# Performance work log

Hardware: AMD Instinct MI355X
Metric: run time of the kernel (lower is better)

Reference implementation:

```python
import jax
import jax.numpy as jnp
import numpy as np
from jax import lax

DELTA = float(np.exp(-2.0))  # rule-creation density threshold


def codebook_lamb(x):
    """Online growing RBF prototype codebook (ALMMo-style) for one layer.

    x: [N, M]. Returns lamb: [N] normalized density of each sample at its
    assigned rule. Faithful (corrected) semantics of Layer.__call__:
      - SEN = squared L2 norm per sample (over feature dim)
      - global mean / mean squared norm over the batch
      - sequential per-sample: if max RBF density over existing rules < exp(-2),
        append a new rule (prototype=c=x, SENc=||x||^2, support=1);
        else update rule_star. Note the source's `support[rule_star] = +1`
        assigns 1, so the running mean update degenerates to c[rule_star]=x,
        SENc[rule_star]=||x||^2 -- replicated here.
      - distances use the (never-updated) prototypes; bandwidth stau uses c.
    """
    N, M = x.shape
    SENx = jnp.sum(x * x, axis=-1)                      # [N]
    gmean = jnp.mean(x, axis=0)                         # [M]
    base = jnp.mean(SENx) - jnp.sum(gmean * gmean)      # SENgmean - SEN(gmean)
    R = N                                               # worst case: one rule/sample

    protos0 = jnp.zeros((R, M), x.dtype)
    pn20 = jnp.zeros((R,), x.dtype)                     # ||proto_r||^2 (carried)
    c0 = jnp.zeros((R, M), x.dtype)
    cn20 = jnp.zeros((R,), x.dtype)                     # ||c_r||^2 (carried)
    SENc0 = jnp.zeros((R,), x.dtype)
    count0 = jnp.int32(0)

    ridx = jnp.arange(R)

    def step(carry, inp):
        protos, pn2, c, cn2, SENc, count = carry
        xi, sxi = inp                                   # [M], scalar
        valid = ridx < count
        stau = (base + SENc - cn2) * 0.5                # [R]
        dist = sxi + pn2 - 2.0 * (protos @ xi)          # [R] ||xi - proto_r||^2
        dens = jnp.where(valid, jnp.exp(-dist / stau), -jnp.inf)
        idx = jnp.argmax(dens)
        vmax = dens[idx]
        new = (count == 0) | (vmax < DELTA)
        slot = jnp.where(new, count, idx)
        # both branches set c/SENc at slot to xi/sxi (support resets to 1)
        c = c.at[slot].set(xi)
        cn2 = cn2.at[slot].set(sxi)
        SENc = SENc.at[slot].set(sxi)
        # only a new rule writes a prototype (OOB scatter when count==R is dropped)
        protos = protos.at[count].set(jnp.where(new, xi, protos[count]))
        pn2 = pn2.at[count].set(jnp.where(new, sxi, pn2[count]))
        count = count + new.astype(count.dtype)
        return (protos, pn2, c, cn2, SENc, count), slot

    (protos, pn2, c, cn2, SENc, count), rules = lax.scan(
        step, (protos0, pn20, c0, cn20, SENc0, count0), (x, SENx)
    )

    # final densities of all samples under all (valid) rules: [R, N]
    stau = (base + SENc - cn2) * 0.5                    # [R]
    dist = SENx[None, :] + pn2[:, None] - 2.0 * (protos @ x.T)
    dens = jnp.where((ridx < count)[:, None], jnp.exp(-dist / stau[:, None]), 0.0)
    dens_xn = dens[rules, jnp.arange(N)]                # density at assigned rule
    lamb = dens_xn / jnp.sum(dens, axis=0)              # normalize over rules
    return lamb


def setup_inputs() -> dict:
    key = jax.random.key(0)
    k = jax.random.split(key, 5)
    N, D_IN, D_H, D_OUT = 2048, 2048, 2048, 1024
    s0 = 1.0 / np.sqrt(D_IN)
    s1 = 1.0 / np.sqrt(D_H)
    return {
        "x": jax.random.normal(k[0], (N, D_IN), jnp.float32),
        "W0": jax.random.normal(k[1], (D_H, D_IN), jnp.float32) * s0,
        "b0": jax.random.normal(k[2], (D_H,), jnp.float32) * s0,
        "W1": jax.random.normal(k[3], (D_OUT, D_H), jnp.float32) * s1,
        "b1": jax.random.normal(k[4], (D_OUT,), jnp.float32) * s1,
    }


def reference(x, W0, b0, W1, b1):
    lambs = []
    h = x
    for W, b in ((W0, b0), (W1, b1)):
        lambs.append(codebook_lamb(h))          # per-layer codebook on layer input
        h = jax.nn.sigmoid(h @ W.T + b)         # torch.nn.Linear + sigmoid
    return h, jnp.stack(lambs)                  # ([N, d_out], [n_layers, N])
```

## Files before the change

### kernel.cpp

```cpp
#include <hip/hip_runtime.h>
#include <cstdint>
#include <cstddef>


#define DELTA_F 0.13533528323661270f
#define MBYTE (1u << 20)

typedef __bf16 bf16;
typedef bf16 bf16x8 __attribute__((ext_vector_type(8)));
typedef bf16 bf16x4 __attribute__((ext_vector_type(4)));
typedef float f32x4 __attribute__((ext_vector_type(4)));

typedef __attribute__((address_space(1))) void as1_void;
typedef __attribute__((address_space(3))) void as3_void;

__device__ __forceinline__ void gload16(const bf16* g, bf16* l) {
  __builtin_amdgcn_global_load_lds((as1_void*)g, (as3_void*)l, 16, 0, 0);
}

__device__ __forceinline__ float wave_reduce(float s) {
  for (int o = 32; o > 0; o >>= 1) s += __shfl_down(s, o, 64);
  return s;
}

template <bool SAME>
__device__ void run_decide_lamb(char* smem, int* e, float* Dens, float* S,
                                float* diagD, float* lambOut) {
  char* s_flag = smem;
  short* s_as = (short*)(smem + 2048);
  short* s_list = (short*)(smem + 6144);
  short* s_re = (short*)(smem + 10240);
  int* scan_ = (int*)(smem + 14336);
  float* rbest = (float*)(smem + 16384);
  int* rbj = (int*)(smem + 18432);
  int* sT = (int*)(smem + 24576);
  int* sReN = (int*)(smem + 24580);
  const int tid = threadIdx.x;
  int cntl = 0;
#pragma unroll
  for (int k = 0; k < 4; ++k) {
    const int i = tid * 4 + k;
    const int ei = SAME ? atomicOr(e + i, 0) : e[i];
    s_flag[i] = (ei == 0);
    if (ei == 0) s_as[i] = (short)i;
    cntl += (ei != 0);
  }
  scan_[tid] = cntl;
  if (tid == 0) sReN[0] = 0;
  __syncthreads();
  for (int off = 1; off < 512; off <<= 1) {
    const int v = scan_[tid];
    const int add = (tid >= off) ? scan_[tid - off] : 0;
    __syncthreads();
    scan_[tid] = v + add;
    __syncthreads();
  }
  int pos = scan_[tid] - cntl;
#pragma unroll
  for (int k = 0; k < 4; ++k) {
    const int i = tid * 4 + k;
    if (!s_flag[i]) s_list[pos++] = (short)i;
  }
  if (tid == 511) sT[0] = scan_[511];
  __syncthreads();
  const int T = sT[0];
  if (SAME && T > 0) __threadfence();
  for (int t = 0; t < T; ++t) {
    const int i = s_list[t];
    const float* di = Dens + (size_t)i * 2048;
    float best = -1.0f;
    int bestj = 0x7fffffff;
    for (int j = tid; j < i; j += 512) {
      if (s_flag[j]) {
        const float d = di[j];
        if (d > best || (d == best && j < bestj)) { best = d; bestj = j; }
      }
    }
    rbest[tid] = best; rbj[tid] = bestj;
    __syncthreads();
    if (tid == 0) {
      float b = -1.0f;
      int bj = 0x7fffffff;
      for (int k = 0; k < 512; ++k)
        if (rbest[k] > b || (rbest[k] == b && rbj[k] < bj)) { b = rbest[k]; bj = rbj[k]; }
      if (b < DELTA_F) { s_flag[i] = 1; s_as[i] = (short)i; }
      else { s_as[i] = (short)bj; s_re[sReN[0]++] = (short)i; }
    }
    __syncthreads();
  }
  const int reN = sReN[0];
#pragma unroll
  for (int k = 0; k < 4; ++k) {
    const int n = k * 512 + tid;
    const int aa = s_as[n];
    const float num = (aa == n)
        ? (SAME ? atomicAdd(diagD + n, 0.f) : diagD[n])
        : Dens[(size_t)n * 2048 + aa];
    float denom = SAME ? atomicAdd(S + n, 0.f) : S[n];
    for (int t = 0; t < reN; ++t) denom -= Dens[(size_t)n * 2048 + s_re[t]];
    lambOut[n] = num / denom;
  }
}

template <bool IS_L0>
__global__ __launch_bounds__(512, 2) void gemm_fused(
    const bf16* __restrict__ A, float* __restrict__ Dens,
    bf16* __restrict__ Hb, float* __restrict__ Fo,
    const float* __restrict__ bias, const float* __restrict__ SENin,
    const float* __restrict__ ninv_p, float* __restrict__ S,
    int* __restrict__ e, float* __restrict__ SENhOut,
    float* __restrict__ colsumH, float* __restrict__ diagD,
    int* __restrict__ cnt, int nblocks, float* __restrict__ lambOut,
    int* __restrict__ flagN, const float* __restrict__ SENh_r,
    const float* __restrict__ colsumH_r, int* __restrict__ e0,
    float* __restrict__ S0, float* __restrict__ diag0,
    float* __restrict__ Dens0, float* __restrict__ lamb0) {
  __shared__ __align__(16) char smemA[49152];
  __shared__ __align__(16) char smemB[49152];
  __shared__ __align__(16) char smemC[49152];
  __shared__ int s_last;
  const int tid = threadIdx.x;

  if (!IS_L0 && blockIdx.x == 24) {
    if (blockIdx.y != 0) return;
    float* r1 = (float*)(smemA + 20480);
    float* r2 = (float*)(smemA + 22528);
    float ssen = 0.f, sg2 = 0.f;
    for (int i = tid; i < 2048; i += 512) ssen += SENh_r[i];
    for (int c = tid; c < 2048; c += 512) {
      const float gm = colsumH_r[c] * (1.f / 2048.f);
      sg2 += gm * gm;
    }
    r1[tid] = ssen; r2[tid] = sg2;
    __syncthreads();
    for (int s = 256; s; s >>= 1) {
      if (tid < s) { r1[tid] += r1[tid + s]; r2[tid] += r2[tid + s]; }
      __syncthreads();
    }
    if (tid == 0) {
      const float stau = 0.5f * (r1[0] * (1.f / 2048.f) - r2[0]);
      atomicExch(flagN, __float_as_int(-1.f / stau));
    }
    __syncthreads();
    run_decide_lamb<false>(smemA, e0, Dens0, S0, diag0, lamb0);
    return;
  }

  int bx, by;
  if (IS_L0) {
    const int lid = blockIdx.x + (blockIdx.y << 5);
    by = lid & 7; bx = lid >> 3;
  } else {
    const int lid = blockIdx.x + blockIdx.y * 25;
    const int xcd = lid & 7, j = lid >> 3;
    by = xcd; bx = j - (j > 3 * (xcd + 1));
  }
  const int m0 = by * 256, n0 = bx * 128;

  const int wave = tid >> 6, lane = tid & 63;
  const int quad = lane >> 4, l16 = lane & 15;
  const int wm = wave >> 1, wn = wave & 1;
  const bool isGram = (n0 < 2048);
  const int sr8 = lane >> 3, slot = lane & 7;
  const int gk = (slot ^ sr8) * 8;
  const bf16* aSrc = A + (size_t)(m0 + wave * 32 + sr8) * 2048 + gk;
  const bf16* bSrc = A + (size_t)(n0 + wave * 16 + sr8) * 2048 + gk;
  char* const aDstA = smemA + wave * 4096;
  char* const bDstA = smemA + 32768 + wave * 2048;
  char* const aDstB = smemB + wave * 4096;
  char* const bDstB = smemB + 32768 + wave * 2048;
  char* const aDstC = smemC + wave * 4096;
  char* const bDstC = smemC + 32768 + wave * 2048;
  const int aB = (wm * 64 + l16) * 128;
  const int bB = 32768 + (wn * 64 + l16) * 128;

#define STAGE(aD, bD, k)                                    \
  do {                                                      \
    gload16(aSrc + (k), (bf16*)(aD));                       \
    gload16(aSrc + 8 * 2048 + (k), (bf16*)((aD) + 1024));   \
    gload16(aSrc + 16 * 2048 + (k), (bf16*)((aD) + 2048));  \
    gload16(aSrc + 24 * 2048 + (k), (bf16*)((aD) + 3072));  \
    gload16(bSrc + (k), (bf16*)(bD));                       \
    gload16(bSrc + 8 * 2048 + (k), (bf16*)((bD) + 1024));   \
  } while (0)

#define COMPUTE(sm)                                                          \
  do {                                                                       \
    _Pragma("unroll") for (int ks = 0; ks < 2; ++ks) {                       \
      bf16x8 af[4], bfr[4];                                                  \
      const int sw = ((ks * 4 + quad) ^ (l16 & 7)) * 16;                     \
      _Pragma("unroll") for (int i = 0; i < 4; ++i)                          \
          af[i] = *(const bf16x8*)((sm) + aB + i * 2048 + sw);               \
      _Pragma("unroll") for (int j = 0; j < 4; ++j)                          \
          bfr[j] = *(const bf16x8*)((sm) + bB + j * 2048 + sw);              \
      _Pragma("unroll") for (int i = 0; i < 4; ++i)                          \
          _Pragma("unroll") for (int j = 0; j < 4; ++j) acc[i][j] =          \
              __builtin_amdgcn_mfma_f32_16x16x32_bf16(af[i], bfr[j],         \
                                                      acc[i][j], 0, 0, 0);   \
    }                                                                        \
  } while (0)

#define WBAR(n)                                                  \
  do {                                                           \
    asm volatile("s_waitcnt vmcnt(" #n ")" ::: "memory");        \
    __builtin_amdgcn_sched_barrier(0);                           \
    __builtin_amdgcn_s_barrier();                                \
    __builtin_amdgcn_sched_barrier(0);                           \
  } while (0)

  f32x4 acc[4][4] = {};
  STAGE(aDstA, bDstA, 0);
  STAGE(aDstB, bDstB, 64);
  for (int k0 = 0; k0 < 1920; k0 += 192) {
    WBAR(6); STAGE(aDstC, bDstC, k0 + 128); COMPUTE(smemA);
    WBAR(6); STAGE(aDstA, bDstA, k0 + 192); COMPUTE(smemB);
    WBAR(6); STAGE(aDstB, bDstB, k0 + 256); COMPUTE(smemC);
  }
  WBAR(6); COMPUTE(smemA);
  WBAR(0); COMPUTE(smemB);
#undef STAGE
#undef COMPUTE
#undef WBAR

  float ninv = 0.f;
  if (isGram) {
    if (IS_L0) ninv = ninv_p[0];
    else {
      int fi;
      while ((fi = atomicOr(flagN, 0)) == 0) {}
      ninv = __int_as_float(fi);
    }
  }

  float colp[4] = {0.f, 0.f, 0.f, 0.f};
#pragma unroll
  for (int i = 0; i < 4; ++i) {
    const int rbase = m0 + wm * 64 + i * 16 + quad * 4;
    if (isGram) {
      const f32x4 si4 = *(const f32x4*)(SENin + rbase);
      float rp[4] = {0.f, 0.f, 0.f, 0.f};
      int er = 0;
#pragma unroll
      for (int j = 0; j < 4; ++j) {
        const f32x4 v = acc[i][j];
        const int col = n0 + wn * 64 + j * 16 + l16;
        const float sj = SENin[col];
#pragma unroll
        for (int r = 0; r < 4; ++r) {
          const float dens = __expf((si4[r] + sj - 2.0f * v[r]) * ninv);
          Dens[(size_t)(rbase + r) * 2048 + col] = dens;
          rp[r] += dens;
          if (col < rbase + r && dens >= DELTA_F) er |= (1 << r);
          if (col == rbase + r) atomicExch(diagD + col, dens);
        }
      }
#pragma unroll
      for (int r = 0; r < 4; ++r) {
        float rv = rp[r];
        rv += __shfl_xor(rv, 1, 64); rv += __shfl_xor(rv, 2, 64);
        rv += __shfl_xor(rv, 4, 64); rv += __shfl_xor(rv, 8, 64);
        if (l16 == 0) atomicAdd(S + rbase + r, rv);
      }
      er |= __shfl_xor(er, 1, 64); er |= __shfl_xor(er, 2, 64);
      er |= __shfl_xor(er, 4, 64); er |= __shfl_xor(er, 8, 64);
      if (l16 == 0 && er) {
#pragma unroll
        for (int r = 0; r < 4; ++r)
          if ((er >> r) & 1) atomicOr(e + rbase + r, 1);
      }
    } else {
      float rn[4] = {0.f, 0.f, 0.f, 0.f};
#pragma unroll
      for (int j = 0; j < 4; ++j) {
        const f32x4 v = acc[i][j];
        const int c2 = n0 - 2048 + wn * 64 + j * 16 + l16;
        const float bv = bias[c2];
#pragma unroll
        for (int r = 0; r < 4; ++r) {
          const float hv = 1.0f / (1.0f + __expf(-(v[r] + bv)));
          if (IS_L0) {
            Hb[(size_t)(rbase + r) * 2048 + c2] = (bf16)hv;
            rn[r] += hv * hv;
            colp[j] += hv;
          } else {
            Fo[(size_t)(rbase + r) * 1024 + c2] = hv;
          }
        }
      }
      if (IS_L0) {
#pragma unroll
        for (int r = 0; r < 4; ++r) {
          float rv = rn[r];
          rv += __shfl_xor(rv, 1, 64); rv += __shfl_xor(rv, 2, 64);
          rv += __shfl_xor(rv, 4, 64); rv += __shfl_xor(rv, 8, 64);
          if (l16 == 0) atomicAdd(SENhOut + rbase + r, rv);
        }
      }
    }
  }
  if (IS_L0 && !isGram) {
#pragma unroll
    for (int j = 0; j < 4; ++j) {
      float cv = colp[j];
      cv += __shfl_xor(cv, 16, 64);
      cv += __shfl_xor(cv, 32, 64);
      if (lane < 16) atomicAdd(colsumH + (n0 - 2048 + wn * 64 + j * 16 + lane), cv);
    }
  }

  if (IS_L0) return;

  __syncthreads();
  if (tid == 0) s_last = (atomicAdd(cnt, 1) == nblocks - 1);
  __syncthreads();
  if (!s_last) return;
  run_decide_lamb<true>(smemA, e, Dens, S, diagD, lambOut);
}

__global__ void f2b_all(const float* __restrict__ x, const float* __restrict__ W0,
                        const float* __restrict__ W1, bf16* __restrict__ xb,
                        bf16* __restrict__ wb0, bf16* __restrict__ wb1,
                        float* __restrict__ SENx, float* __restrict__ bins,
                        int* __restrict__ cntF, float* __restrict__ scal) {
  const int b = blockIdx.x, tid = threadIdx.x;
  const int wave = tid >> 6, lane = tid & 63;
  __shared__ float ws[8][4];
  __shared__ float red1[256], red2[256];
  __shared__ int s_last;
  if (b < 256) {
    const int r0 = b * 8;
    f32x4 c0 = {0.f, 0.f, 0.f, 0.f}, c1 = {0.f, 0.f, 0.f, 0.f};
    for (int r = 0; r < 8; ++r) {
      const float* src = x + (size_t)(r0 + r) * 2048;
      bf16* dst = xb + (size_t)(r0 + r) * 2048;
      f32x4 v0 = *(const f32x4*)(src + tid * 4);
      f32x4 v1 = *(const f32x4*)(src + 1024 + tid * 4);
      bf16x4 o0, o1;
      o0.x = (bf16)v0.x; o0.y = (bf16)v0.y; o0.z = (bf16)v0.z; o0.w = (bf16)v0.w;
      o1.x = (bf16)v1.x; o1.y = (bf16)v1.y; o1.z = (bf16)v1.z; o1.w = (bf16)v1.w;
      *(bf16x4*)(dst + tid * 4) = o0;
      *(bf16x4*)(dst + 1024 + tid * 4) = o1;
      c0 += v0; c1 += v1;
      float rn = v0.x * v0.x + v0.y * v0.y + v0.z * v0.z + v0.w * v0.w +
                 v1.x * v1.x + v1.y * v1.y + v1.z * v1.z + v1.w * v1.w;
      rn = wave_reduce(rn);
      if (lane == 0) ws[r][wave] = rn;
    }
    __syncthreads();
    if (tid < 8)
      atomicExch(SENx + r0 + tid, ws[tid][0] + ws[tid][1] + ws[tid][2] + ws[tid][3]);
    float* bin = bins + (size_t)(b & 15) * 2048;
    atomicAdd(bin + tid * 4 + 0, c0.x); atomicAdd(bin + tid * 4 + 1, c0.y);
    atomicAdd(bin + tid * 4 + 2, c0.z); atomicAdd(bin + tid * 4 + 3, c0.w);
    atomicAdd(bin + 1024 + tid * 4 + 0, c1.x); atomicAdd(bin + 1024 + tid * 4 + 1, c1.y);
    atomicAdd(bin + 1024 + tid * 4 + 2, c1.z); atomicAdd(bin + 1024 + tid * 4 + 3, c1.w);
  } else if (b < 512) {
    const size_t base = (size_t)(b - 256) * 16384;
    for (int c = tid * 4; c < 16384; c += 1024) {
      f32x4 v = *(const f32x4*)(W0 + base + c);
      bf16x4 o;
      o.x = (bf16)v.x; o.y = (bf16)v.y; o.z = (bf16)v.z; o.w = (bf16)v.w;
      *(bf16x4*)(wb0 + base + c) = o;
    }
  } else {
    const size_t base = (size_t)(b - 512) * 16384;
    for (int c = tid * 4; c < 16384; c += 1024) {
      f32x4 v = *(const f32x4*)(W1 + base + c);
      bf16x4 o;
      o.x = (bf16)v.x; o.y = (bf16)v.y; o.z = (bf16)v.z; o.w = (bf16)v.w;
      *(bf16x4*)(wb1 + base + c) = o;
    }
  }

  __syncthreads();
  if (tid == 0) s_last = (atomicAdd(cntF, 1) == 639);
  __syncthreads();
  if (!s_last) return;
  float ssen = 0.f;
  for (int i = tid; i < 2048; i += 256) ssen += atomicAdd(SENx + i, 0.f);
  float sg2 = 0.f;
  for (int c = tid; c < 2048; c += 256) {
    float cs = 0.f;
#pragma unroll
    for (int p = 0; p < 16; ++p) cs += atomicAdd(bins + (size_t)p * 2048 + c, 0.f);
    const float gm = cs * (1.f / 2048.f);
    sg2 += gm * gm;
  }
  red1[tid] = ssen; red2[tid] = sg2;
  __syncthreads();
  for (int s = 128; s; s >>= 1) {
    if (tid < s) { red1[tid] += red1[tid + s]; red2[tid] += red2[tid + s]; }
    __syncthreads();
  }
  if (tid == 0) {
    const float stau = 0.5f * (red1[0] * (1.f / 2048.f) - red2[0]);
    scal[0] = stau;
    scal[1] = -1.f / stau;
  }
}

extern "C" void kernel_launch(void* const* d_in, const int* in_sizes, int n_in,
                              void* d_out, int out_size, void* d_ws, size_t ws_size,
                              hipStream_t stream) {
  const float* x = (const float*)d_in[0];
  const float* W0 = (const float*)d_in[1];
  const float* b0 = (const float*)d_in[2];
  const float* W1 = (const float*)d_in[3];
  const float* b1 = (const float*)d_in[4];
  float* out = (float*)d_out;

  char* w = (char*)d_ws;
  bf16* xb = (bf16*)(w);
  bf16* wb0 = (bf16*)(w + 8 * MBYTE);
  bf16* hb = (bf16*)(w + 16 * MBYTE);
  bf16* wb1 = (bf16*)(w + 24 * MBYTE);
  float* Dens0 = (float*)(w + 28 * MBYTE);
  float* Dens1 = (float*)(w);
  float* SENx = (float*)(w + 44 * MBYTE);
  float* scal = SENx + 2048;
  float* zre = scal + 16;
  float* bins = zre;
  float* SENh = bins + 16 * 2048;
  float* colsumH = SENh + 2048;
  float* S0 = colsumH + 2048;
  float* S1 = S0 + 2048;
  float* diagD0 = S1 + 2048;
  float* diagD1 = diagD0 + 2048;
  int* e0 = (int*)(diagD1 + 2048);
  int* e1 = e0 + 2048;
  int* cntF = e1 + 2048;
  int* cnt1 = cntF + 1;
  int* flagN = cnt1 + 1;
  const size_t zwords = 16 * 2048 + 8 * 2048 + 16;

  float* lamb0 = out + (size_t)2048 * 1024;
  float* lamb1 = lamb0 + 2048;

  hipMemsetAsync(zre, 0, zwords * 4, stream);
  f2b_all<<<640, 256, 0, stream>>>(x, W0, W1, xb, wb0, wb1, SENx, bins, cntF, scal);
  gemm_fused<true><<<dim3(32, 8), 512, 0, stream>>>(
      xb, Dens0, hb, nullptr, b0, SENx, scal + 1, S0, e0, SENh, colsumH,
      diagD0, nullptr, 0, nullptr,
      nullptr, nullptr, nullptr, nullptr, nullptr, nullptr, nullptr, nullptr);
  gemm_fused<false><<<dim3(25, 8), 512, 0, stream>>>(
      hb, Dens1, nullptr, out, b1, SENh, nullptr, S1, e1, nullptr, nullptr,
      diagD1, cnt1, 192, lamb1,
      flagN, SENh, colsumH, e0, S0, diagD0, Dens0, lamb0);
}
```

Baseline: 189.9 us.

## Load GEMM B operand directly into registers instead of staging through LDS

The B tile is no longer staged in LDS. Each wave now loads its B fragments straight from global memory into double-buffered registers, one phase ahead, while A keeps its three-stage LDS pipeline and the LDS buffers shrink to 32KB each. The aim is to cut LDS traffic and the LDS read instructions for B, and to lower LDS use. In exchange it adds register pressure, and B is fetched redundantly from global/L2, since each row is loaded by every wave that uses it rather than once per block.

```diff
diff --git a/kernel.cpp b/kernel.cpp
--- a/kernel.cpp
+++ b/kernel.cpp
@@ -115,9 +115,9 @@
     const float* __restrict__ colsumH_r, int* __restrict__ e0,
     float* __restrict__ S0, float* __restrict__ diag0,
     float* __restrict__ Dens0, float* __restrict__ lamb0) {
-  __shared__ __align__(16) char smemA[49152];
-  __shared__ __align__(16) char smemB[49152];
-  __shared__ __align__(16) char smemC[49152];
+  __shared__ __align__(16) char smemA[32768];
+  __shared__ __align__(16) char smemB[32768];
+  __shared__ __align__(16) char smemC[32768];
   __shared__ int s_last;
   const int tid = threadIdx.x;
 
@@ -164,38 +164,52 @@
   const int sr8 = lane >> 3, slot = lane & 7;
   const int gk = (slot ^ sr8) * 8;
   const bf16* aSrc = A + (size_t)(m0 + wave * 32 + sr8) * 2048 + gk;
-  const bf16* bSrc = A + (size_t)(n0 + wave * 16 + sr8) * 2048 + gk;
   char* const aDstA = smemA + wave * 4096;
-  char* const bDstA = smemA + 32768 + wave * 2048;
   char* const aDstB = smemB + wave * 4096;
-  char* const bDstB = smemB + 32768 + wave * 2048;
   char* const aDstC = smemC + wave * 4096;
-  char* const bDstC = smemC + 32768 + wave * 2048;
   const int aB = (wm * 64 + l16) * 128;
-  const int bB = 32768 + (wn * 64 + l16) * 128;
-
-#define STAGE(aD, bD, k)                                    \
+  const int sw0 = ((0 * 4 + quad) ^ (l16 & 7)) * 16;
+  const int sw1 = ((1 * 4 + quad) ^ (l16 & 7)) * 16;
+  const bf16* bRow0 = A + (size_t)(n0 + wn * 64 + 0 * 16 + l16) * 2048 + quad * 8;
+  const bf16* bRow1 = A + (size_t)(n0 + wn * 64 + 1 * 16 + l16) * 2048 + quad * 8;
+  const bf16* bRow2 = A + (size_t)(n0 + wn * 64 + 2 * 16 + l16) * 2048 + quad * 8;
+  const bf16* bRow3 = A + (size_t)(n0 + wn * 64 + 3 * 16 + l16) * 2048 + quad * 8;
+
+  bf16x8 bsA[8], bsB[8];
+  f32x4 acc[4][4] = {};
+
+#define STAGEA(aD, k)                                       \
   do {                                                      \
     gload16(aSrc + (k), (bf16*)(aD));                       \
     gload16(aSrc + 8 * 2048 + (k), (bf16*)((aD) + 1024));   \
     gload16(aSrc + 16 * 2048 + (k), (bf16*)((aD) + 2048));  \
     gload16(aSrc + 24 * 2048 + (k), (bf16*)((aD) + 3072));  \
-    gload16(bSrc + (k), (bf16*)(bD));                       \
-    gload16(bSrc + 8 * 2048 + (k), (bf16*)((bD) + 1024));   \
   } while (0)
 
-#define COMPUTE(sm)                                                          \
+#define LOADB(dst, kk)                                              \
+  do {                                                              \
+    dst[0] = *(const bf16x8*)(bRow0 + (kk));                        \
+    dst[1] = *(const bf16x8*)(bRow1 + (kk));                        \
+    dst[2] = *(const bf16x8*)(bRow2 + (kk));                        \
+    dst[3] = *(const bf16x8*)(bRow3 + (kk));                        \
+    dst[4] = *(const bf16x8*)(bRow0 + (kk) + 32);                   \
+    dst[5] = *(const bf16x8*)(bRow1 + (kk) + 32);                   \
+    dst[6] = *(const bf16x8*)(bRow2 + (kk) + 32);                   \
+    dst[7] = *(const bf16x8*)(bRow3 + (kk) + 32);                   \
+  } while (0)
+
+#define SBV() __builtin_amdgcn_sched_barrier(0x38F)
+
+#define COMPUTE(sm, bs)                                                      \
   do {                                                                       \
     _Pragma("unroll") for (int ks = 0; ks < 2; ++ks) {                       \
-      bf16x8 af[4], bfr[4];                                                  \
-      const int sw = ((ks * 4 + quad) ^ (l16 & 7)) * 16;                     \
+      bf16x8 af[4];                                                          \
+      const int sw = ks ? sw1 : sw0;                                         \
       _Pragma("unroll") for (int i = 0; i < 4; ++i)                          \
           af[i] = *(const bf16x8*)((sm) + aB + i * 2048 + sw);               \
-      _Pragma("unroll") for (int j = 0; j < 4; ++j)                          \
-          bfr[j] = *(const bf16x8*)((sm) + bB + j * 2048 + sw);              \
       _Pragma("unroll") for (int i = 0; i < 4; ++i)                          \
           _Pragma("unroll") for (int j = 0; j < 4; ++j) acc[i][j] =          \
-              __builtin_amdgcn_mfma_f32_16x16x32_bf16(af[i], bfr[j],         \
+              __builtin_amdgcn_mfma_f32_16x16x32_bf16(af[i], bs[ks * 4 + j], \
                                                       acc[i][j], 0, 0, 0);   \
     }                                                                        \
   } while (0)
@@ -208,19 +222,41 @@
     __builtin_amdgcn_sched_barrier(0);                           \
   } while (0)
 
-  f32x4 acc[4][4] = {};
-  STAGE(aDstA, bDstA, 0);
-  STAGE(aDstB, bDstB, 64);
-  for (int k0 = 0; k0 < 1920; k0 += 192) {
-    WBAR(6); STAGE(aDstC, bDstC, k0 + 128); COMPUTE(smemA);
-    WBAR(6); STAGE(aDstA, bDstA, k0 + 192); COMPUTE(smemB);
-    WBAR(6); STAGE(aDstB, bDstB, k0 + 256); COMPUTE(smemC);
-  }
-  WBAR(6); COMPUTE(smemA);
-  WBAR(0); COMPUTE(smemB);
-#undef STAGE
+#define PHASE(smC_, bsCur, bsNxt, kB, kA, aD)     \
+  do {                                            \
+    WBAR(4);                                      \
+    LOADB(bsNxt, (kB));                           \
+    SBV();                                        \
+    STAGEA(aD, (kA));                             \
+    SBV();                                        \
+    COMPUTE(smC_, bsCur);                         \
+  } while (0)
+
+  LOADB(bsA, 0);
+  SBV();
+  STAGEA(aDstA, 0);
+  SBV();
+  STAGEA(aDstB, 64);
+  for (int k0 = 0; k0 < 1920; k0 += 384) {
+    PHASE(smemA, bsA, bsB, k0 + 64,  k0 + 128, aDstC);
+    PHASE(smemB, bsB, bsA, k0 + 128, k0 + 192, aDstA);
+    PHASE(smemC, bsA, bsB, k0 + 192, k0 + 256, aDstB);
+    PHASE(smemA, bsB, bsA, k0 + 256, k0 + 320, aDstC);
+    PHASE(smemB, bsA, bsB, k0 + 320, k0 + 384, aDstA);
+    PHASE(smemC, bsB, bsA, k0 + 384, k0 + 448, aDstB);
+  }
+  WBAR(4);
+  LOADB(bsB, 1984);
+  SBV();
+  COMPUTE(smemA, bsA);
+  WBAR(0);
+  COMPUTE(smemB, bsB);
+#undef STAGEA
+#undef LOADB
 #undef COMPUTE
 #undef WBAR
+#undef PHASE
+#undef SBV
 
   float ninv = 0.f;
   if (isGram) {
```

Measured after the change: 288.4 us. +51.9%, slower.

## Split K across wave pairs with larger per-wave tiles and LDS reduction

Applied to the files above, without the earlier changes.

Reassigns the eight waves so that pairs split each 64-wide K chunk (kg selects the 32-wide half). Each wave now computes a 128x64 output sub-tile (8x4 MFMA accumulators) instead of 64x64. The pairs' partial accumulators are then summed through LDS in four rounds before the unchanged epilogue. This raises fragment reuse per LDS load (8 A and 4 B fragments feed 32 MFMAs) but doubles accumulator registers, adds LDS exchange rounds with barriers, and leaves half the waves idle during the epilogue.

```diff
diff --git a/kernel.cpp b/kernel.cpp
--- a/kernel.cpp
+++ b/kernel.cpp
@@ -159,7 +159,7 @@
 
   const int wave = tid >> 6, lane = tid & 63;
   const int quad = lane >> 4, l16 = lane & 15;
-  const int wm = wave >> 1, wn = wave & 1;
+  const int kg = wave & 1, wm = (wave >> 1) & 1, wn = (wave >> 2) & 1;
   const bool isGram = (n0 < 2048);
   const int sr8 = lane >> 3, slot = lane & 7;
   const int gk = (slot ^ sr8) * 8;
@@ -171,8 +171,9 @@
   char* const bDstB = smemB + 32768 + wave * 2048;
   char* const aDstC = smemC + wave * 4096;
   char* const bDstC = smemC + 32768 + wave * 2048;
-  const int aB = (wm * 64 + l16) * 128;
+  const int aB = (wm * 128 + l16) * 128;
   const int bB = 32768 + (wn * 64 + l16) * 128;
+  const int sw = ((kg * 4 + quad) ^ (l16 & 7)) * 16;
 
 #define STAGE(aD, bD, k)                                    \
   do {                                                      \
@@ -186,18 +187,15 @@
 
 #define COMPUTE(sm)                                                          \
   do {                                                                       \
-    _Pragma("unroll") for (int ks = 0; ks < 2; ++ks) {                       \
-      bf16x8 af[4], bfr[4];                                                  \
-      const int sw = ((ks * 4 + quad) ^ (l16 & 7)) * 16;                     \
-      _Pragma("unroll") for (int i = 0; i < 4; ++i)                          \
-          af[i] = *(const bf16x8*)((sm) + aB + i * 2048 + sw);               \
+    bf16x8 af[8], bfr[4];                                                    \
+    _Pragma("unroll") for (int j = 0; j < 4; ++j)                            \
+        bfr[j] = *(const bf16x8*)((sm) + bB + j * 2048 + sw);                \
+    _Pragma("unroll") for (int i = 0; i < 8; ++i)                            \
+        af[i] = *(const bf16x8*)((sm) + aB + i * 2048 + sw);                 \
+    _Pragma("unroll") for (int i = 0; i < 8; ++i)                            \
       _Pragma("unroll") for (int j = 0; j < 4; ++j)                          \
-          bfr[j] = *(const bf16x8*)((sm) + bB + j * 2048 + sw);              \
-      _Pragma("unroll") for (int i = 0; i < 4; ++i)                          \
-          _Pragma("unroll") for (int j = 0; j < 4; ++j) acc[i][j] =          \
-              __builtin_amdgcn_mfma_f32_16x16x32_bf16(af[i], bfr[j],         \
-                                                      acc[i][j], 0, 0, 0);   \
-    }                                                                        \
+        acc[i][j] = __builtin_amdgcn_mfma_f32_16x16x32_bf16(af[i], bfr[j],   \
+                                                            acc[i][j], 0, 0, 0); \
   } while (0)
 
 #define WBAR(n)                                                  \
@@ -208,7 +206,7 @@
     __builtin_amdgcn_sched_barrier(0);                           \
   } while (0)
 
-  f32x4 acc[4][4] = {};
+  f32x4 acc[8][4] = {};
   STAGE(aDstA, bDstA, 0);
   STAGE(aDstB, bDstB, 64);
   for (int k0 = 0; k0 < 1920; k0 += 192) {
@@ -233,72 +231,88 @@
   }
 
   float colp[4] = {0.f, 0.f, 0.f, 0.f};
-#pragma unroll
-  for (int i = 0; i < 4; ++i) {
-    const int rbase = m0 + wm * 64 + i * 16 + quad * 4;
-    if (isGram) {
-      const f32x4 si4 = *(const f32x4*)(SENin + rbase);
-      float rp[4] = {0.f, 0.f, 0.f, 0.f};
-      int er = 0;
-#pragma unroll
-      for (int j = 0; j < 4; ++j) {
-        const f32x4 v = acc[i][j];
-        const int col = n0 + wn * 64 + j * 16 + l16;
-        const float sj = SENin[col];
-#pragma unroll
-        for (int r = 0; r < 4; ++r) {
-          const float dens = __expf((si4[r] + sj - 2.0f * v[r]) * ninv);
-          Dens[(size_t)(rbase + r) * 2048 + col] = dens;
-          rp[r] += dens;
-          if (col < rbase + r && dens >= DELTA_F) er |= (1 << r);
-          if (col == rbase + r) atomicExch(diagD + col, dens);
-        }
-      }
-#pragma unroll
-      for (int r = 0; r < 4; ++r) {
-        float rv = rp[r];
-        rv += __shfl_xor(rv, 1, 64); rv += __shfl_xor(rv, 2, 64);
-        rv += __shfl_xor(rv, 4, 64); rv += __shfl_xor(rv, 8, 64);
-        if (l16 == 0) atomicAdd(S + rbase + r, rv);
-      }
-      er |= __shfl_xor(er, 1, 64); er |= __shfl_xor(er, 2, 64);
-      er |= __shfl_xor(er, 4, 64); er |= __shfl_xor(er, 8, 64);
-      if (l16 == 0 && er) {
-#pragma unroll
-        for (int r = 0; r < 4; ++r)
-          if ((er >> r) & 1) atomicOr(e + rbase + r, 1);
-      }
-    } else {
-      float rn[4] = {0.f, 0.f, 0.f, 0.f};
-#pragma unroll
-      for (int j = 0; j < 4; ++j) {
-        const f32x4 v = acc[i][j];
-        const int c2 = n0 - 2048 + wn * 64 + j * 16 + l16;
-        const float bv = bias[c2];
-#pragma unroll
-        for (int r = 0; r < 4; ++r) {
-          const float hv = 1.0f / (1.0f + __expf(-(v[r] + bv)));
+  char* const ex = smemA + (wn * 2 + wm) * 8192;
+#pragma unroll
+  for (int round = 0; round < 4; ++round) {
+    __syncthreads();
+    if (kg == 1) {
+#pragma unroll
+      for (int ii = 0; ii < 2; ++ii)
+#pragma unroll
+        for (int j = 0; j < 4; ++j)
+          *(f32x4*)(ex + (ii * 4 + j) * 1024 + lane * 16) = acc[round * 2 + ii][j];
+    }
+    __syncthreads();
+    if (kg == 0) {
+#pragma unroll
+      for (int ii = 0; ii < 2; ++ii) {
+        const int i = round * 2 + ii;
+        const int rbase = m0 + wm * 128 + i * 16 + quad * 4;
+        if (isGram) {
+          const f32x4 si4 = *(const f32x4*)(SENin + rbase);
+          float rp[4] = {0.f, 0.f, 0.f, 0.f};
+          int er = 0;
+#pragma unroll
+          for (int j = 0; j < 4; ++j) {
+            f32x4 v = acc[i][j] + *(const f32x4*)(ex + (ii * 4 + j) * 1024 + lane * 16);
+            const int col = n0 + wn * 64 + j * 16 + l16;
+            const float sj = SENin[col];
+#pragma unroll
+            for (int r = 0; r < 4; ++r) {
+              const float dens = __expf((si4[r] + sj - 2.0f * v[r]) * ninv);
+              Dens[(size_t)(rbase + r) * 2048 + col] = dens;
+              rp[r] += dens;
+              if (col < rbase + r && dens >= DELTA_F) er |= (1 << r);
+              if (col == rbase + r) atomicExch(diagD + col, dens);
+            }
+          }
+#pragma unroll
+          for (int r = 0; r < 4; ++r) {
+            float rv = rp[r];
+            rv += __shfl_xor(rv, 1, 64); rv += __shfl_xor(rv, 2, 64);
+            rv += __shfl_xor(rv, 4, 64); rv += __shfl_xor(rv, 8, 64);
+            if (l16 == 0) atomicAdd(S + rbase + r, rv);
+          }
+          er |= __shfl_xor(er, 1, 64); er |= __shfl_xor(er, 2, 64);
+          er |= __shfl_xor(er, 4, 64); er |= __shfl_xor(er, 8, 64);
+          if (l16 == 0 && er) {
+#pragma unroll
+            for (int r = 0; r < 4; ++r)
+              if ((er >> r) & 1) atomicOr(e + rbase + r, 1);
+          }
+        } else {
+          float rn[4] = {0.f, 0.f, 0.f, 0.f};
+#pragma unroll
+          for (int j = 0; j < 4; ++j) {
+            f32x4 v = acc[i][j] + *(const f32x4*)(ex + (ii * 4 + j) * 1024 + lane * 16);
+            const int c2 = n0 - 2048 + wn * 64 + j * 16 + l16;
+            const float bv = bias[c2];
+#pragma unroll
+            for (int r = 0; r < 4; ++r) {
+              const float hv = 1.0f / (1.0f + __expf(-(v[r] + bv)));
+              if (IS_L0) {
+                Hb[(size_t)(rbase + r) * 2048 + c2] = (bf16)hv;
+                rn[r] += hv * hv;
+                colp[j] += hv;
+              } else {
+                Fo[(size_t)(rbase + r) * 1024 + c2] = hv;
+              }
+            }
+          }
           if (IS_L0) {
-            Hb[(size_t)(rbase + r) * 2048 + c2] = (bf16)hv;
-            rn[r] += hv * hv;
-            colp[j] += hv;
-          } else {
-            Fo[(size_t)(rbase + r) * 1024 + c2] = hv;
+#pragma unroll
+            for (int r = 0; r < 4; ++r) {
+              float rv = rn[r];
+              rv += __shfl_xor(rv, 1, 64); rv += __shfl_xor(rv, 2, 64);
+              rv += __shfl_xor(rv, 4, 64); rv += __shfl_xor(rv, 8, 64);
+              if (l16 == 0) atomicAdd(SENhOut + rbase + r, rv);
+            }
           }
         }
       }
-      if (IS_L0) {
-#pragma unroll
-        for (int r = 0; r < 4; ++r) {
-          float rv = rn[r];
-          rv += __shfl_xor(rv, 1, 64); rv += __shfl_xor(rv, 2, 64);
-          rv += __shfl_xor(rv, 4, 64); rv += __shfl_xor(rv, 8, 64);
-          if (l16 == 0) atomicAdd(SENhOut + rbase + r, rv);
-        }
-      }
-    }
-  }
-  if (IS_L0 && !isGram) {
+    }
+  }
+  if (IS_L0 && !isGram && kg == 0) {
 #pragma unroll
     for (int j = 0; j < 4; ++j) {
       float cv = colp[j];
```

After: 207.4 us. +9.2%, slower.
